# Kernel tuning notes

Hardware: AMD Instinct MI355X
Metric: run time of the kernel (lower is better)

Reference implementation:

```python
import jax, jax.numpy as jnp
import numpy as np

# hparams (match init_kwargs)
EXP_LOW_BOUND = -8.0          # clip scores-max to [low_bound, 0]
EXP_CLIP_AND_SUBTRACT = True  # subtract exp(low_bound) from clipped tensor before exp
EXP_LINEAR_GRADIENT = 0.0     # 0 -> use true exp on the clipped/shifted tensor
EXP_SUM_HIGH_BOUND = 1024.0   # clamp the softmax denominator
RECIP_LINEAR_GRADIENT = 0.0   # 0 -> exact reciprocal
RECIP_LOW_BOUND = 0.0

B, S, H, D = 4, 1024, 16, 64


def _approx_exp(x):
    # exponential() from the source
    if EXP_LOW_BOUND != 0:
        x = jnp.clip(x, EXP_LOW_BOUND, 0.0)
    if EXP_CLIP_AND_SUBTRACT:
        x = x - np.float32(np.exp(EXP_LOW_BOUND))
    if EXP_LINEAR_GRADIENT:
        return jnp.clip(x * np.float32(EXP_LINEAR_GRADIENT) + 1.0, 0.0, 1.0)
    return jnp.exp(x)


def _approx_recip(x):
    # reciprocal() from the source
    if RECIP_LINEAR_GRADIENT != 0:
        g = np.float32(RECIP_LINEAR_GRADIENT)
        return jnp.clip((1.0 + g) - g * x, RECIP_LOW_BOUND, 1.0)
    return 1.0 / x


def _custom_softmax(a):
    # softmax() with exp_hparams / reciprocal_hparams path, norm over last axis
    amax = jnp.max(a, axis=-1, keepdims=True)
    amax = jnp.where(jnp.isfinite(amax), amax, 0.0)
    asubmax = a - amax
    approx_exp = _approx_exp(asubmax)                       # [B,H,Sq,Sk]
    asumexp = jnp.sum(approx_exp, axis=-1, keepdims=True)   # [B,H,Sq,1]
    if EXP_SUM_HIGH_BOUND:
        sum_low_bound = 1.0
        if EXP_LOW_BOUND != 0 and EXP_CLIP_AND_SUBTRACT:
            sum_low_bound = 1.0 - float(np.exp(EXP_LOW_BOUND))
        asumexp = jnp.clip(asumexp, sum_low_bound, EXP_SUM_HIGH_BOUND)
    return approx_exp * _approx_recip(asumexp)


def setup_inputs() -> dict:
    key = jax.random.key(0)
    kq, kk, kv = jax.random.split(key, 3)
    return {
        "query": jax.random.normal(kq, (B, S, H, D), dtype=jnp.float32),
        "key": jax.random.normal(kk, (B, S, H, D), dtype=jnp.float32),
        "value": jax.random.normal(kv, (B, S, H, D), dtype=jnp.float32),
    }


def reference(query, key, value):
    depth = query.shape[-1]
    q = query * (1.0 / np.sqrt(depth)).astype(np.float32)
    # scores: [B, H, Sq, Sk]
    scores = jnp.einsum("bqhd,bkhd->bhqk", q, key)
    weights = _custom_softmax(scores).astype(query.dtype)
    # output: [B, Sq, H, D]
    return jnp.einsum("bhqk,bkhd->bqhd", weights, value)
```

## Files before the change

### kernel.cpp

```cpp
#include <hip/hip_runtime.h>

#define SS 1024
#define HH 16
#define DD 64

typedef short bf16x8 __attribute__((ext_vector_type(8)));
typedef float f32x4 __attribute__((ext_vector_type(4)));

__device__ __forceinline__ unsigned pk2(float a, float b) {
    unsigned ua = __float_as_uint(a) + 0x8000u;
    unsigned ub = __float_as_uint(b) + 0x8000u;
    return (ub & 0xffff0000u) | (ua >> 16);
}
__device__ __forceinline__ unsigned short f2bf(float a) {
    return (unsigned short)((__float_as_uint(a) + 0x8000u) >> 16);
}
__device__ __forceinline__ f32x4 mfma16(bf16x8 a, bf16x8 b, f32x4 c) {
    return __builtin_amdgcn_mfma_f32_16x16x32_bf16(a, b, c, 0, 0, 0);
}
__device__ __forceinline__ int sig5(int x) {
    int a = (x >> 4) & 1, qs = (x >> 2) & 3, b2 = x & 3;
    return ((qs ^ (b2 >> 1)) << 3) | (a << 2) | b2;
}
__device__ __forceinline__ unsigned swz1k(unsigned o) {
    return o ^ (((o >> 7) & 7u) << 4);
}

__device__ __forceinline__ void step32v(bf16x8 K0, bf16x8 K1, bf16x8 K2, bf16x8 K3,
                                        bf16x8 V0, bf16x8 V1, bf16x8 V2, bf16x8 V3,
                                        const bf16x8 qf[2][2],
                                        f32x4 oacc[2][4], float su[2]) {
    const f32x4 zero = {0.f, 0.f, 0.f, 0.f};
    const float LOG2E = 1.44269504f;
    f32x4 S[2][2];
    S[0][0] = mfma16(K1, qf[0][1], mfma16(K0, qf[0][0], zero));
    S[1][0] = mfma16(K1, qf[1][1], mfma16(K0, qf[1][0], zero));
    S[0][1] = mfma16(K3, qf[0][1], mfma16(K2, qf[0][0], zero));
    S[1][1] = mfma16(K3, qf[1][1], mfma16(K2, qf[1][0], zero));
    #pragma unroll
    for (int s = 0; s < 2; ++s) {
        unsigned P0[2], P1[2];
        #pragma unroll
        for (int ct = 0; ct < 2; ++ct) {
            float e0 = __builtin_amdgcn_exp2f(S[s][ct][0] * LOG2E);
            float e1 = __builtin_amdgcn_exp2f(S[s][ct][1] * LOG2E);
            float e2 = __builtin_amdgcn_exp2f(S[s][ct][2] * LOG2E);
            float e3 = __builtin_amdgcn_exp2f(S[s][ct][3] * LOG2E);
            su[s] += (e0 + e1) + (e2 + e3);
            P0[ct] = pk2(e0, e1);
            P1[ct] = pk2(e2, e3);
        }
        union { uint4 u; bf16x8 f; } pf;
        pf.u.x = P0[0];
        pf.u.y = (unsigned)__shfl_xor((int)P1[0], 16);
        pf.u.z = P0[1];
        pf.u.w = (unsigned)__shfl_xor((int)P1[1], 16);
        #pragma unroll
        for (int dt = 0; dt < 4; ++dt) {
            bf16x8 vv = dt == 0 ? V0 : dt == 1 ? V1 : dt == 2 ? V2 : V3;
            oacc[s][dt] = mfma16(vv, pf.f, oacc[s][dt]);
        }
    }
}

__global__ __launch_bounds__(256, 2)
void attn_fused(const float* __restrict__ q, const float* __restrict__ k,
                const float* __restrict__ v, float* __restrict__ out) {
    __shared__ __align__(16) unsigned short ldsbuf[16384];

    const int t = threadIdx.x, lane = t & 63, w = t >> 6;
    const int n16 = lane & 15, quad = lane >> 4;
    const int bx = blockIdx.x;
    const int bh = bx & 63, qt = bx >> 6;
    const int h = bh & 15, b = bh >> 4;
    const int qbase = qt * 128 + w * 32;

    const int kx = t >> 3, khalf = (t >> 2) & 1, ku = t & 3;
    const int kf = ((kx >> 4) & 1) * 2 + khalf;
    const unsigned kwoff = (unsigned)(kf * 1024)
                         + swz1k((unsigned)((kx & 15) * 64 + ku * 16));
    const int ksig = sig5(kx);
    const bool vact = (t & 3) == 0;
    const int vtid = t >> 2, vo = vtid >> 4, vvc = vtid & 15;

    const float4* kbase = (const float4*)k + ((size_t)(b * SS) * HH + h) * 16
                        + khalf * 8 + 2 * ku;
    const float4* vbase = (const float4*)v + ((size_t)(b * SS + vo * 8) * HH + h) * 16
                        + vvc;

    bf16x8 qf[2][2];
    #pragma unroll
    for (int s = 0; s < 2; ++s)
      #pragma unroll
      for (int ks = 0; ks < 2; ++ks) {
        const float* p = q + (((size_t)(b * SS + qbase + s * 16 + n16) * HH + h) * DD)
                           + ks * 32 + quad * 8;
        float4 x = ((const float4*)p)[0];
        float4 y = ((const float4*)p)[1];
        bf16x8 f;
        f[0] = (short)f2bf(x.x * 0.125f); f[1] = (short)f2bf(x.y * 0.125f);
        f[2] = (short)f2bf(x.z * 0.125f); f[3] = (short)f2bf(x.w * 0.125f);
        f[4] = (short)f2bf(y.x * 0.125f); f[5] = (short)f2bf(y.y * 0.125f);
        f[6] = (short)f2bf(y.z * 0.125f); f[7] = (short)f2bf(y.w * 0.125f);
        qf[s][ks] = f;
      }

    f32x4 oacc[2][4];
    #pragma unroll
    for (int s = 0; s < 2; ++s)
      #pragma unroll
      for (int dt = 0; dt < 4; ++dt) oacc[s][dt] = f32x4{0.f, 0.f, 0.f, 0.f};
    float su[2] = {0.f, 0.f};

    const unsigned okK = swz1k(((unsigned)n16 << 6) | ((unsigned)quad << 4));
    const unsigned okV = swz1k(((unsigned)quad << 8) | ((unsigned)n16 << 4));

#define ISSUE(c, kr, vr) do {                                                    \
    const float4* ks_ = kbase + (size_t)((c) * 32 + ksig) * (HH * 16);           \
    kr[0] = ks_[0]; kr[1] = ks_[1];                                              \
    if (vact) {                                                                  \
        const float4* vs_ = vbase + (size_t)(c) * 32 * (HH * 16);                \
        _Pragma("unroll")                                                        \
        for (int kk_ = 0; kk_ < 8; ++kk_) vr[kk_] = vs_[kk_ * (HH * 16)];        \
    }                                                                            \
} while (0)

#define WRITE(slot, kr, vr) do {                                                 \
    char* sb_ = (char*)ldsbuf + (slot) * 8192;                                   \
    uint4 kv_;                                                                   \
    kv_.x = pk2(kr[0].x, kr[0].y); kv_.y = pk2(kr[0].z, kr[0].w);                \
    kv_.z = pk2(kr[1].x, kr[1].y); kv_.w = pk2(kr[1].z, kr[1].w);                \
    *(uint4*)(sb_ + kwoff) = kv_;                                                \
    if (vact) {                                                                  \
        const float* fr_ = (const float*)vr;                                     \
        _Pragma("unroll")                                                        \
        for (int cc_ = 0; cc_ < 4; ++cc_) {                                      \
            const int d_ = 4 * vvc + cc_;                                        \
            uint4 q4_;                                                           \
            q4_.x = pk2(fr_[0*4+cc_], fr_[1*4+cc_]);                             \
            q4_.y = pk2(fr_[2*4+cc_], fr_[3*4+cc_]);                             \
            q4_.z = pk2(fr_[4*4+cc_], fr_[5*4+cc_]);                             \
            q4_.w = pk2(fr_[6*4+cc_], fr_[7*4+cc_]);                             \
            *(uint4*)(sb_ + 4096 + (d_ >> 4) * 1024 +                            \
                      swz1k((unsigned)(vo * 256 + (d_ & 15) * 16))) = q4_;       \
        }                                                                        \
    }                                                                            \
} while (0)

#define BAR asm volatile("s_waitcnt lgkmcnt(0)\n\ts_barrier" ::: "memory")

#define COMPUTE(slot) do {                                                       \
    const char* cb_ = (const char*)ldsbuf + (slot) * 8192;                       \
    bf16x8 K0 = *(const bf16x8*)(cb_ + okK);                                     \
    bf16x8 K1 = *(const bf16x8*)(cb_ + okK + 1024);                              \
    bf16x8 K2 = *(const bf16x8*)(cb_ + okK + 2048);                              \
    bf16x8 K3 = *(const bf16x8*)(cb_ + okK + 3072);                              \
    bf16x8 V0 = *(const bf16x8*)(cb_ + okV + 4096);                              \
    bf16x8 V1 = *(const bf16x8*)(cb_ + okV + 5120);                              \
    bf16x8 V2 = *(const bf16x8*)(cb_ + okV + 6144);                              \
    bf16x8 V3 = *(const bf16x8*)(cb_ + okV + 7168);                              \
    step32v(K0, K1, K2, K3, V0, V1, V2, V3, qf, oacc, su);                       \
} while (0)

    float4 krA[2], vrA[8], krB[2], vrB[8];

    ISSUE(0, krA, vrA);
    WRITE(0, krA, vrA);
    ISSUE(1, krB, vrB);
    BAR;

    #pragma unroll 1
    for (int it2 = 0; it2 < 16; ++it2) {
        const int it = it2 * 2;
        WRITE((it + 1) & 3, krB, vrB);
        { const int c_ = (it + 2 < 32) ? it + 2 : 31; ISSUE(c_, krA, vrA); }
        BAR;
        COMPUTE(it & 3);
        WRITE((it + 2) & 3, krA, vrA);
        { const int c_ = (it + 3 < 32) ? it + 3 : 31; ISSUE(c_, krB, vrB); }
        BAR;
        COMPUTE((it + 1) & 3);
    }
#undef ISSUE
#undef WRITE
#undef BAR
#undef COMPUTE

    #pragma unroll
    for (int s = 0; s < 2; ++s) {
        su[s] += __shfl_xor(su[s], 16);
        su[s] += __shfl_xor(su[s], 32);
    }
    #pragma unroll
    for (int s = 0; s < 2; ++s) {
        float sc = 1.0f / su[s];
        #pragma unroll
        for (int dt = 0; dt < 4; ++dt) {
            float4 val;
            val.x = oacc[s][dt][0] * sc;
            val.y = oacc[s][dt][1] * sc;
            val.z = oacc[s][dt][2] * sc;
            val.w = oacc[s][dt][3] * sc;
            size_t off = ((size_t)(b * SS + qbase + s * 16 + n16) * HH + h) * DD
                       + dt * 16 + quad * 4;
            *(float4*)&out[off] = val;
        }
    }
}

extern "C" void kernel_launch(void* const* d_in, const int* in_sizes, int n_in,
                              void* d_out, int out_size, void* d_ws, size_t ws_size,
                              hipStream_t stream) {
    const float* q = (const float*)d_in[0];
    const float* k = (const float*)d_in[1];
    const float* v = (const float*)d_in[2];
    float* o = (float*)d_out;
    (void)d_ws; (void)ws_size;
    hipLaunchKernelGGL(attn_fused, dim3(512), dim3(256), 0, stream, q, k, v, o);
}
```

Measured before the change: 123.7 us.

## Split key dimension across two blocks and combine partial attention outputs

The attention kernel now splits the 1024 keys into two halves handled by separate blocks, so the grid doubles from 512 to 1024 and launch bounds allow four blocks per CU. Each block writes unnormalized partial outputs and row sums to workspace, and a second combine kernel adds the halves and normalizes. This aims to raise occupancy and fill more CUs. The cost is an extra kernel launch plus writing and reading about 64MB of fp32 partials through the workspace. Summing partials without max rescaling is valid because the kernel already uses exp without a running max.

```diff
diff --git a/kernel.cpp b/kernel.cpp
--- a/kernel.cpp
+++ b/kernel.cpp
@@ -63,17 +63,20 @@
     }
 }
 
-__global__ __launch_bounds__(256, 2)
-void attn_fused(const float* __restrict__ q, const float* __restrict__ k,
-                const float* __restrict__ v, float* __restrict__ out) {
+__global__ __launch_bounds__(256, 4)
+void attn_partial(const float* __restrict__ q, const float* __restrict__ k,
+                  const float* __restrict__ v, float* __restrict__ wso,
+                  float* __restrict__ wss) {
     __shared__ __align__(16) unsigned short ldsbuf[16384];
 
     const int t = threadIdx.x, lane = t & 63, w = t >> 6;
     const int n16 = lane & 15, quad = lane >> 4;
     const int bx = blockIdx.x;
-    const int bh = bx & 63, qt = bx >> 6;
+    const int bh = bx & 63, rest = bx >> 6;
+    const int qt = rest >> 1, half = rest & 1;
     const int h = bh & 15, b = bh >> 4;
     const int qbase = qt * 128 + w * 32;
+    const int cbase = half * 16;
 
     const int kx = t >> 3, khalf = (t >> 2) & 1, ku = t & 3;
     const int kf = ((kx >> 4) & 1) * 2 + khalf;
@@ -115,13 +118,14 @@
     const unsigned okK = swz1k(((unsigned)n16 << 6) | ((unsigned)quad << 4));
     const unsigned okV = swz1k(((unsigned)quad << 8) | ((unsigned)n16 << 4));
 
-#define ISSUE(c, kr, vr) do {                                                    \
-    const float4* ks_ = kbase + (size_t)((c) * 32 + ksig) * (HH * 16);           \
+#define ISSUE(ci, kr, vr) do {                                                   \
+    const int c_ = cbase + (ci);                                                 \
+    const float4* ks_ = kbase + (size_t)(c_ * 32 + ksig) * 256;                  \
     kr[0] = ks_[0]; kr[1] = ks_[1];                                              \
     if (vact) {                                                                  \
-        const float4* vs_ = vbase + (size_t)(c) * 32 * (HH * 16);                \
+        const float4* vs_ = vbase + (size_t)c_ * 8192;                           \
         _Pragma("unroll")                                                        \
-        for (int kk_ = 0; kk_ < 8; ++kk_) vr[kk_] = vs_[kk_ * (HH * 16)];        \
+        for (int kk_ = 0; kk_ < 8; ++kk_) vr[kk_] = vs_[kk_ * 256];              \
     }                                                                            \
 } while (0)
 
@@ -170,16 +174,16 @@
     BAR;
 
     #pragma unroll 1
-    for (int it2 = 0; it2 < 16; ++it2) {
-        const int it = it2 * 2;
-        WRITE((it + 1) & 3, krB, vrB);
-        { const int c_ = (it + 2 < 32) ? it + 2 : 31; ISSUE(c_, krA, vrA); }
+    for (int it2 = 0; it2 < 8; ++it2) {
+        const int i = it2 * 2;
+        WRITE((i + 1) & 3, krB, vrB);
+        { const int ci = (i + 2 < 16) ? i + 2 : 15; ISSUE(ci, krA, vrA); }
         BAR;
-        COMPUTE(it & 3);
-        WRITE((it + 2) & 3, krA, vrA);
-        { const int c_ = (it + 3 < 32) ? it + 3 : 31; ISSUE(c_, krB, vrB); }
+        COMPUTE(i & 3);
+        WRITE((i + 2) & 3, krA, vrA);
+        { const int ci = (i + 3 < 16) ? i + 3 : 15; ISSUE(ci, krB, vrB); }
         BAR;
-        COMPUTE((it + 1) & 3);
+        COMPUTE((i + 1) & 3);
     }
 #undef ISSUE
 #undef WRITE
@@ -191,21 +195,39 @@
         su[s] += __shfl_xor(su[s], 16);
         su[s] += __shfl_xor(su[s], 32);
     }
-    #pragma unroll
-    for (int s = 0; s < 2; ++s) {
-        float sc = 1.0f / su[s];
-        #pragma unroll
-        for (int dt = 0; dt < 4; ++dt) {
-            float4 val;
-            val.x = oacc[s][dt][0] * sc;
-            val.y = oacc[s][dt][1] * sc;
-            val.z = oacc[s][dt][2] * sc;
-            val.w = oacc[s][dt][3] * sc;
-            size_t off = ((size_t)(b * SS + qbase + s * 16 + n16) * HH + h) * DD
-                       + dt * 16 + quad * 4;
-            *(float4*)&out[off] = val;
-        }
-    }
+    const int pb = bh * 8 + qt;
+    float4* wo4 = (float4*)wso + (size_t)half * 1048576u;
+    #pragma unroll
+    for (int s = 0; s < 2; ++s)
+      #pragma unroll
+      for (int dt = 0; dt < 4; ++dt) {
+        float4 val;
+        val.x = oacc[s][dt][0]; val.y = oacc[s][dt][1];
+        val.z = oacc[s][dt][2]; val.w = oacc[s][dt][3];
+        wo4[((size_t)pb * 128 + w * 32 + s * 16 + n16) * 16 + dt * 4 + quad] = val;
+      }
+    if (quad == 0) {
+        wss[half * 65536 + pb * 128 + w * 32 + n16]      = su[0];
+        wss[half * 65536 + pb * 128 + w * 32 + 16 + n16] = su[1];
+    }
+}
+
+__global__ __launch_bounds__(256)
+void combine_kernel(const float* __restrict__ wso, const float* __restrict__ wss,
+                    float* __restrict__ out) {
+    const unsigned gi = blockIdx.x * 256u + threadIdx.x;
+    const unsigned row = gi >> 4, d4 = gi & 15;
+    const float4* o4 = (const float4*)wso;
+    float4 a = o4[gi];
+    float4 c = o4[gi + 1048576u];
+    float sc = 1.0f / (wss[row] + wss[row + 65536]);
+    const unsigned pb = row >> 7, r128 = row & 127;
+    const unsigned bh = pb >> 3, qt = pb & 7;
+    const unsigned b = bh >> 4, h = bh & 15;
+    float4 val;
+    val.x = (a.x + c.x) * sc; val.y = (a.y + c.y) * sc;
+    val.z = (a.z + c.z) * sc; val.w = (a.w + c.w) * sc;
+    ((float4*)out)[(((size_t)b * SS + qt * 128 + r128) * HH + h) * 16 + d4] = val;
 }
 
 extern "C" void kernel_launch(void* const* d_in, const int* in_sizes, int n_in,
@@ -215,6 +237,8 @@
     const float* k = (const float*)d_in[1];
     const float* v = (const float*)d_in[2];
     float* o = (float*)d_out;
-    (void)d_ws; (void)ws_size;
-    hipLaunchKernelGGL(attn_fused, dim3(512), dim3(256), 0, stream, q, k, v, o);
-}
+    float* wso = (float*)d_ws;
+    float* wss = wso + 8388608;
+    hipLaunchKernelGGL(attn_partial, dim3(1024), dim3(256), 0, stream, q, k, v, wso, wss);
+    hipLaunchKernelGGL(combine_kernel, dim3(4096), dim3(256), 0, stream, wso, wss, o);
+}
```

After: 450.7 us. 3.64x slower.

## Batch two K/V chunks per barrier and raise wave priority during MFMA compute

Applied to the files above, without the earlier changes.

Restructures the main loop so each iteration writes two staged K/V chunks to LDS, issues global loads for the next two chunks, and then uses a single barrier before computing both chunks. This halves the number of barriers per chunk pair. It also wraps the compute phase in s_setprio so MFMA-heavy waves are scheduled ahead of others. The changed ordering means an LDS slot written in one iteration must not still be read by lagging waves from the previous iteration. With a single barrier per iteration that safety depends on the 4-slot ring, so slot reuse across iterations needs care.

```diff
diff --git a/kernel.cpp b/kernel.cpp
--- a/kernel.cpp
+++ b/kernel.cpp
@@ -115,13 +115,14 @@
     const unsigned okK = swz1k(((unsigned)n16 << 6) | ((unsigned)quad << 4));
     const unsigned okV = swz1k(((unsigned)quad << 8) | ((unsigned)n16 << 4));
 
-#define ISSUE(c, kr, vr) do {                                                    \
-    const float4* ks_ = kbase + (size_t)((c) * 32 + ksig) * (HH * 16);           \
+#define ISSUE(ci, kr, vr) do {                                                   \
+    const int c_ = (ci);                                                         \
+    const float4* ks_ = kbase + (size_t)(c_ * 32 + ksig) * 256;                  \
     kr[0] = ks_[0]; kr[1] = ks_[1];                                              \
     if (vact) {                                                                  \
-        const float4* vs_ = vbase + (size_t)(c) * 32 * (HH * 16);                \
+        const float4* vs_ = vbase + (size_t)c_ * 8192;                           \
         _Pragma("unroll")                                                        \
-        for (int kk_ = 0; kk_ < 8; ++kk_) vr[kk_] = vs_[kk_ * (HH * 16)];        \
+        for (int kk_ = 0; kk_ < 8; ++kk_) vr[kk_] = vs_[kk_ * 256];              \
     }                                                                            \
 } while (0)
 
@@ -165,21 +166,20 @@
     float4 krA[2], vrA[8], krB[2], vrB[8];
 
     ISSUE(0, krA, vrA);
-    WRITE(0, krA, vrA);
     ISSUE(1, krB, vrB);
-    BAR;
 
     #pragma unroll 1
-    for (int it2 = 0; it2 < 16; ++it2) {
-        const int it = it2 * 2;
-        WRITE((it + 1) & 3, krB, vrB);
-        { const int c_ = (it + 2 < 32) ? it + 2 : 31; ISSUE(c_, krA, vrA); }
+    for (int j = 0; j < 16; ++j) {
+        const int i = j * 2;
+        WRITE(i & 3, krA, vrA);
+        WRITE((i + 1) & 3, krB, vrB);
+        { const int ci = (i + 2 < 32) ? i + 2 : 31; ISSUE(ci, krA, vrA); }
+        { const int ci = (i + 3 < 32) ? i + 3 : 31; ISSUE(ci, krB, vrB); }
         BAR;
-        COMPUTE(it & 3);
-        WRITE((it + 2) & 3, krA, vrA);
-        { const int c_ = (it + 3 < 32) ? it + 3 : 31; ISSUE(c_, krB, vrB); }
-        BAR;
-        COMPUTE((it + 1) & 3);
+        __builtin_amdgcn_s_setprio(1);
+        COMPUTE(i & 3);
+        COMPUTE((i + 1) & 3);
+        __builtin_amdgcn_s_setprio(0);
     }
 #undef ISSUE
 #undef WRITE
```

Measured after the change: 119.3 us. 3.6% less time.
